# Kernel tuning notes

Measured on AMD Instinct MI355X. Metric: run time of the kernel, lower is better.

## Reference

```python
import jax, jax.numpy as jnp
import numpy as np

BATCH, FIELD0, EMB = 1024, 32, 64
LAYER_SIZES = (128, 128, 128)  # split_half=True -> hidden field sizes [32, 64, 64]


def setup_inputs() -> dict:
    key = jax.random.key(0)
    ks = jax.random.split(key, 7)
    x = jax.random.normal(ks[0], (BATCH, FIELD0, EMB), dtype=jnp.float32)
    # Conv1D(kernel_size=1) weights: (in_channels=f0*fi, filters=layer_size), plus bias.
    field_sizes = [FIELD0]
    params = {}
    for i, size in enumerate(LAYER_SIZES):
        fi = field_sizes[-1]
        fan_in = FIELD0 * fi
        scale = 1.0 / np.sqrt(fan_in)
        params[f"W{i}"] = jax.random.normal(ks[1 + 2 * i], (fan_in, size), dtype=jnp.float32) * scale
        params[f"b{i}"] = jnp.zeros((size,), dtype=jnp.float32)
        field_sizes.append(size // 2 if i != len(LAYER_SIZES) - 1 else size)
    return {"x": x, **params}


def reference(x, W0, b0, W1, b1, W2, b2):
    # CIN: outer product + 1x1 conv (a matmul over the flattened field-pair axis)
    # fused as a single bilinear contraction per layer:
    #   cur[b,k,e] = sum_{i,j} x[b,i,e] * hidden[b,j,e] * W[i,j,k] + b[k]
    Ws = [(W0, b0), (W1, b1), (W2, b2)]
    f0 = x.shape[1]
    hidden = x
    final_outputs = []
    n_layers = len(Ws)
    for idx, (W, b) in enumerate(Ws):
        fi = hidden.shape[1]
        Wr = W.reshape(f0, fi, W.shape[-1])  # channel m = i*fi + j (row-major reshape)
        cur = jnp.einsum('bie,bje,ijk->bke', x, hidden, Wr) + b[None, :, None]
        # activation=None -> linear
        if idx != n_layers - 1:
            half = cur.shape[1] // 2
            hidden, direct = cur[:, :half, :], cur[:, half:, :]
        else:
            direct = cur
        final_outputs.append(direct)
    result = jnp.concatenate(final_outputs, axis=1)  # (B, 64+64+128, E)
    return jnp.sum(result, axis=-1)  # (B, 256)
```

## Files before the change

kernel.cpp:

```cpp
#include <hip/hip_runtime.h>
#include <cstdint>


typedef _Float16 half8  __attribute__((ext_vector_type(8)));
typedef _Float16 half4_ __attribute__((ext_vector_type(4)));
typedef _Float16 half2_ __attribute__((ext_vector_type(2)));
typedef float    f32x4  __attribute__((ext_vector_type(4)));

__global__ void pack_w_all(const float* __restrict__ W0, _Float16* __restrict__ Wt0,
                           const float* __restrict__ W1, _Float16* __restrict__ Wt1,
                           const float* __restrict__ W2, _Float16* __restrict__ Wt2)
{
    __shared__ _Float16 ldsT[128 * 33];
    const int blk = blockIdx.x, t = threadIdx.x;
    const float* W;
    _Float16* Wt;
    int c, fi;
    if (blk < 32)       { W = W0; Wt = Wt0; c = blk;      fi = 32; }
    else if (blk < 96)  { W = W1; Wt = Wt1; c = blk - 32; fi = 64; }
    else                { W = W2; Wt = Wt2; c = blk - 96; fi = 64; }

    for (int p = t; p < 32 * 128; p += 256) {
        int kk = p >> 7, m = p & 127;
        ldsT[m * 33 + kk] = (_Float16)W[(size_t)(kk * fi + c) * 128 + m];
    }
    __syncthreads();
    int m = t >> 1, kk0 = (t & 1) * 16;
    half8 v0, v1;
#pragma unroll
    for (int i = 0; i < 8; ++i) {
        v0[i] = ldsT[m * 33 + kk0 + i];
        v1[i] = ldsT[m * 33 + kk0 + 8 + i];
    }
    *(half8*)(Wt + (size_t)c * 4096 + t * 16)     = v0;
    *(half8*)(Wt + (size_t)c * 4096 + t * 16 + 8) = v1;
}

template<int NCH>
__device__ __forceinline__ void kloop_t(f32x4 (&acc)[4][4],
    const _Float16* __restrict__ WtL, const _Float16* __restrict__ hB,
    const half8 (&xF)[4], int lr, int q)
{
#pragma unroll
    for (int mt = 0; mt < 4; ++mt)
#pragma unroll
        for (int nt = 0; nt < 4; ++nt)
            acc[mt][nt] = f32x4{0.0f, 0.0f, 0.0f, 0.0f};

    const _Float16* aG = WtL + lr * 32 + q * 8;

    half8 afA[4], afB[4];
    _Float16 xsA[4], xsB[4];

    auto pf = [&](half8* af, _Float16* xs, int cc) {
        const _Float16* ag = aG + (size_t)cc * 4096;
#pragma unroll
        for (int mt = 0; mt < 4; ++mt)
            af[mt] = *(const half8*)(ag + mt * 512);
#pragma unroll
        for (int nt = 0; nt < 4; ++nt)
            xs[nt] = hB[cc * 72 + nt * 16 + lr];
    };
    auto cp = [&](half8* af, _Float16* xs) {
        __builtin_amdgcn_s_setprio(1);
#pragma unroll
        for (int nt = 0; nt < 4; ++nt) {
            half2_ xv2 = {xs[nt], xs[nt]};
            half8 xv8 = __builtin_shufflevector(xv2, xv2, 0, 1, 0, 1, 0, 1, 0, 1);
            half8 bf = xF[nt] * xv8;
#pragma unroll
            for (int mt = 0; mt < 4; ++mt)
                acc[mt][nt] = __builtin_amdgcn_mfma_f32_16x16x32_f16(
                    af[mt], bf, acc[mt][nt], 0, 0, 0);
        }
        __builtin_amdgcn_s_setprio(0);
    };

    pf(afA, xsA, 0);
    for (int cc = 0; cc < NCH; cc += 2) {
        pf(afB, xsB, cc + 1);
        cp(afA, xsA);
        if (cc + 2 < NCH) pf(afA, xsA, cc + 2);
        cp(afB, xsB);
    }
}

__global__ __launch_bounds__(256, 2)
void cin_fused(const float* __restrict__ x,
               const _Float16* __restrict__ Wt0,
               const _Float16* __restrict__ Wt1,
               const float* __restrict__ bs0,
               const float* __restrict__ bs1,
               _Float16* __restrict__ S0,
               _Float16* __restrict__ S1,
               _Float16* __restrict__ S2)
{
    __shared__ alignas(16) char smem[57344];
    const int t = threadIdx.x, lane = t & 63, w = t >> 6;
    const int lr = lane & 15, q = lane >> 4;
    const int batch = blockIdx.x * 4 + w;

    _Float16* hB = (_Float16*)(smem + w * 14336);
    _Float16* xT = (_Float16*)(smem + w * 14336 + 9216);

    {
        const float4* xv = (const float4*)(x + (size_t)batch * 2048);
#pragma unroll
        for (int s = 0; s < 8; ++s) {
            int p4 = lane + s * 64;
            float4 v = xv[p4];
            int idx = p4 * 4, i = idx >> 6, e0 = idx & 63;
            _Float16 h0 = (_Float16)v.x, h1 = (_Float16)v.y;
            _Float16 h2 = (_Float16)v.z, h3 = (_Float16)v.w;
            half4_ pk = {h0, h1, h2, h3};
            *(half4_*)(hB + i * 72 + e0) = pk;
            xT[(e0 + 0) * 40 + i] = h0;
            xT[(e0 + 1) * 40 + i] = h1;
            xT[(e0 + 2) * 40 + i] = h2;
            xT[(e0 + 3) * 40 + i] = h3;
        }
    }

    half8 xF[4];
#pragma unroll
    for (int nt = 0; nt < 4; ++nt)
        xF[nt] = *(const half8*)(xT + (nt * 16 + lr) * 40 + q * 8);
    const half8 aF00 = *(const half8*)(hB + lr * 72 + q * 8);
    const half8 aF01 = *(const half8*)(hB + lr * 72 + q * 8 + 32);
    const half8 aF10 = *(const half8*)(hB + (16 + lr) * 72 + q * 8);
    const half8 aF11 = *(const half8*)(hB + (16 + lr) * 72 + q * 8 + 32);

    f32x4 acc[4][4];

    auto epi = [&](const float* bs) {
#pragma unroll
        for (int mt = 0; mt < 4; ++mt) {
            const int jb = mt * 16 + q * 4;
            const float b0f = bs[jb + 0], b1f = bs[jb + 1];
            const float b2f = bs[jb + 2], b3f = bs[jb + 3];
#pragma unroll
            for (int nt = 0; nt < 4; ++nt) {
                const int e = nt * 16 + lr;
                hB[(jb + 0) * 72 + e] = (_Float16)(acc[mt][nt][0] + b0f);
                hB[(jb + 1) * 72 + e] = (_Float16)(acc[mt][nt][1] + b1f);
                hB[(jb + 2) * 72 + e] = (_Float16)(acc[mt][nt][2] + b2f);
                hB[(jb + 3) * 72 + e] = (_Float16)(acc[mt][nt][3] + b3f);
            }
        }
    };

    auto sgemm = [&](int fi, _Float16* Sdst) {
        const int njt = fi >> 4;
        _Float16* Sb = Sdst + (size_t)batch * (32 * fi);
        for (int jt = 0; jt < njt; ++jt) {
            half8 bv0 = *(const half8*)(hB + (jt * 16 + lr) * 72 + q * 8);
            half8 bv1 = *(const half8*)(hB + (jt * 16 + lr) * 72 + q * 8 + 32);
            f32x4 sa = {0.0f, 0.0f, 0.0f, 0.0f};
            sa = __builtin_amdgcn_mfma_f32_16x16x32_f16(aF00, bv0, sa, 0, 0, 0);
            sa = __builtin_amdgcn_mfma_f32_16x16x32_f16(aF01, bv1, sa, 0, 0, 0);
            f32x4 sb = {0.0f, 0.0f, 0.0f, 0.0f};
            sb = __builtin_amdgcn_mfma_f32_16x16x32_f16(aF10, bv0, sb, 0, 0, 0);
            sb = __builtin_amdgcn_mfma_f32_16x16x32_f16(aF11, bv1, sb, 0, 0, 0);
            half4_ v0, v1;
#pragma unroll
            for (int r = 0; r < 4; ++r) { v0[r] = (_Float16)sa[r]; v1[r] = (_Float16)sb[r]; }
            *(half4_*)(Sb + (jt * 16 + lr) * 32 + q * 4)      = v0;
            *(half4_*)(Sb + (jt * 16 + lr) * 32 + 16 + q * 4) = v1;
        }
    };

    sgemm(32, S0);
    kloop_t<32>(acc, Wt0, hB, xF, lr, q);
    epi(bs0);
    sgemm(64, S1);
    kloop_t<64>(acc, Wt1, hB, xF, lr, q);
    epi(bs1);
    sgemm(64, S2);
}

__global__ __launch_bounds__(256, 2)
void cin_direct(const _Float16* __restrict__ S0v, const _Float16* __restrict__ S1v,
                const _Float16* __restrict__ S2v,
                const _Float16* __restrict__ Wt0, const _Float16* __restrict__ Wt1,
                const _Float16* __restrict__ Wt2,
                const float* __restrict__ bs0, const float* __restrict__ bs1,
                const float* __restrict__ bs2,
                float* __restrict__ out)
{
    __shared__ f32x4 red[3][64];
    const int t = threadIdx.x, lane = t & 63, kh = t >> 6;
    const int lr = lane & 15, q = lane >> 4;
    const int task = blockIdx.x;

    const _Float16 *S, *Wt;
    const float* bias;
    int fan, nch, dm0, ob, idx;
    if (task < 256)      { S = S0v; Wt = Wt0; bias = bs0; fan = 1024; nch = 32; dm0 = 64; ob = 0;   idx = task; }
    else if (task < 512) { S = S1v; Wt = Wt1; bias = bs1; fan = 2048; nch = 64; dm0 = 64; ob = 64;  idx = task - 256; }
    else                 { S = S2v; Wt = Wt2; bias = bs2; fan = 2048; nch = 64; dm0 = 0;  ob = 128; idx = task - 512; }
    const int bt = idx & 63, kt = idx >> 6;
    const int bbase = bt * 16;
    const int hq = nch >> 2, c0 = kh * hq;

    const _Float16* aG = Wt + (size_t)(dm0 + kt * 16 + lr) * 32 + q * 8
                            + (size_t)c0 * 4096;
    const _Float16* bG = S + (size_t)(bbase + lr) * fan + q * 8 + c0 * 32;

    f32x4 acc = {0.0f, 0.0f, 0.0f, 0.0f};
    half8 aA = *(const half8*)(aG);
    half8 bA = *(const half8*)(bG);
    for (int c = 0; c < hq; c += 2) {
        half8 aB = *(const half8*)(aG + (size_t)(c + 1) * 4096);
        half8 bB = *(const half8*)(bG + (c + 1) * 32);
        acc = __builtin_amdgcn_mfma_f32_16x16x32_f16(aA, bA, acc, 0, 0, 0);
        if (c + 2 < hq) {
            aA = *(const half8*)(aG + (size_t)(c + 2) * 4096);
            bA = *(const half8*)(bG + (c + 2) * 32);
        }
        acc = __builtin_amdgcn_mfma_f32_16x16x32_f16(aB, bB, acc, 0, 0, 0);
    }
    if (kh != 0) red[kh - 1][lane] = acc;
    __syncthreads();
    if (kh == 0) {
#pragma unroll
        for (int p = 0; p < 3; ++p) {
            f32x4 o = red[p][lane];
#pragma unroll
            for (int r = 0; r < 4; ++r) acc[r] += o[r];
        }
#pragma unroll
        for (int r = 0; r < 4; ++r) {
            int kl = kt * 16 + q * 4 + r;
            out[(size_t)(bbase + lr) * 256 + ob + kl]
                = acc[r] + 64.0f * bias[dm0 + kl];
        }
    }
}

extern "C" void kernel_launch(void* const* d_in, const int* in_sizes, int n_in,
                              void* d_out, int out_size, void* d_ws, size_t ws_size,
                              hipStream_t stream)
{
    const float* x  = (const float*)d_in[0];
    const float* W0 = (const float*)d_in[1];
    const float* b0 = (const float*)d_in[2];
    const float* W1 = (const float*)d_in[3];
    const float* b1 = (const float*)d_in[4];
    const float* W2 = (const float*)d_in[5];
    const float* b2 = (const float*)d_in[6];
    float* out = (float*)d_out;

    char* ws = (char*)d_ws;
    _Float16* Wt0 = (_Float16*)(ws + 0);
    _Float16* Wt1 = (_Float16*)(ws + 262144);
    _Float16* Wt2 = (_Float16*)(ws + 786432);
    _Float16* S0  = (_Float16*)(ws + 1310720);
    _Float16* S1  = (_Float16*)(ws + 3407872);
    _Float16* S2  = (_Float16*)(ws + 7602176);
    (void)in_sizes; (void)n_in; (void)out_size; (void)ws_size;

    hipLaunchKernelGGL(pack_w_all, dim3(160), dim3(256), 0, stream,
                       W0, Wt0, W1, Wt1, W2, Wt2);

    hipLaunchKernelGGL(cin_fused, dim3(256), dim3(256), 0, stream,
                       x, Wt0, Wt1, b0, b1, S0, S1, S2);

    hipLaunchKernelGGL(cin_direct, dim3(1024), dim3(256), 0, stream,
                       S0, S1, S2, Wt0, Wt1, Wt2, b0, b1, b2, out);
}
```

Before: 123.8 us.

## Split each batch's CIN recurrence across four waves with split-K LDS reduction

Before, each wave handled one batch element by itself. Now a whole 256-thread block handles one batch, and the grid grows from 256 to 1024 blocks. Each wave takes a quarter of the K channels in the hidden-layer GEMM, and the partial accumulators are summed through LDS in fp16 with several block barriers. The s-GEMM tiles are also spread across the waves. The aim is to raise parallelism and occupancy, since shared memory per block drops, at the cost of extra synchronisation and reduction traffic, plus some precision loss from fp16 partial sums.

After: 117.5 us. 1.05x faster.

```diff
diff --git a/kernel.cpp b/kernel.cpp
--- a/kernel.cpp
+++ b/kernel.cpp
@@ -39,7 +39,7 @@
 template<int NCH>
 __device__ __forceinline__ void kloop_t(f32x4 (&acc)[4][4],
     const _Float16* __restrict__ WtL, const _Float16* __restrict__ hB,
-    const half8 (&xF)[4], int lr, int q)
+    const half8 (&xF)[4], int lr, int q, int w)
 {
 #pragma unroll
     for (int mt = 0; mt < 4; ++mt)
@@ -47,7 +47,10 @@
         for (int nt = 0; nt < 4; ++nt)
             acc[mt][nt] = f32x4{0.0f, 0.0f, 0.0f, 0.0f};
 
-    const _Float16* aG = WtL + lr * 32 + q * 8;
+    constexpr int HC = NCH / 4;
+    const int c0 = w * HC;
+    const _Float16* aG = WtL + (size_t)c0 * 4096 + lr * 32 + q * 8;
+    const _Float16* hP = hB + (size_t)c0 * 72 + lr;
 
     half8 afA[4], afB[4];
     _Float16 xsA[4], xsB[4];
@@ -57,9 +60,10 @@
 #pragma unroll
         for (int mt = 0; mt < 4; ++mt)
             af[mt] = *(const half8*)(ag + mt * 512);
+        const _Float16* hh = hP + cc * 72;
 #pragma unroll
         for (int nt = 0; nt < 4; ++nt)
-            xs[nt] = hB[cc * 72 + nt * 16 + lr];
+            xs[nt] = hh[nt * 16];
     };
     auto cp = [&](half8* af, _Float16* xs) {
         __builtin_amdgcn_s_setprio(1);
@@ -77,10 +81,10 @@
     };
 
     pf(afA, xsA, 0);
-    for (int cc = 0; cc < NCH; cc += 2) {
+    for (int cc = 0; cc < HC; cc += 2) {
         pf(afB, xsB, cc + 1);
         cp(afA, xsA);
-        if (cc + 2 < NCH) pf(afA, xsA, cc + 2);
+        if (cc + 2 < HC) pf(afA, xsA, cc + 2);
         cp(afB, xsB);
     }
 }
@@ -95,19 +99,20 @@
                _Float16* __restrict__ S1,
                _Float16* __restrict__ S2)
 {
-    __shared__ alignas(16) char smem[57344];
+    __shared__ alignas(16) char smem[26624];
+    _Float16* xT   = (_Float16*)smem;
+    _Float16* hB   = (_Float16*)(smem + 5120);
+    _Float16* XC16 = (_Float16*)(smem + 14336);
+
     const int t = threadIdx.x, lane = t & 63, w = t >> 6;
     const int lr = lane & 15, q = lane >> 4;
-    const int batch = blockIdx.x * 4 + w;
-
-    _Float16* hB = (_Float16*)(smem + w * 14336);
-    _Float16* xT = (_Float16*)(smem + w * 14336 + 9216);
+    const int b = blockIdx.x;
 
     {
-        const float4* xv = (const float4*)(x + (size_t)batch * 2048);
-#pragma unroll
-        for (int s = 0; s < 8; ++s) {
-            int p4 = lane + s * 64;
+        const float4* xv = (const float4*)(x + (size_t)b * 2048);
+#pragma unroll
+        for (int s = 0; s < 2; ++s) {
+            int p4 = t + s * 256;
             float4 v = xv[p4];
             int idx = p4 * 4, i = idx >> 6, e0 = idx & 63;
             _Float16 h0 = (_Float16)v.x, h1 = (_Float16)v.y;
@@ -120,61 +125,103 @@
             xT[(e0 + 3) * 40 + i] = h3;
         }
     }
+    __syncthreads();
 
     half8 xF[4];
 #pragma unroll
     for (int nt = 0; nt < 4; ++nt)
         xF[nt] = *(const half8*)(xT + (nt * 16 + lr) * 40 + q * 8);
-    const half8 aF00 = *(const half8*)(hB + lr * 72 + q * 8);
-    const half8 aF01 = *(const half8*)(hB + lr * 72 + q * 8 + 32);
-    const half8 aF10 = *(const half8*)(hB + (16 + lr) * 72 + q * 8);
-    const half8 aF11 = *(const half8*)(hB + (16 + lr) * 72 + q * 8 + 32);
+    const int it = w & 1;
+    const half8 aF0 = *(const half8*)(hB + (it * 16 + lr) * 72 + q * 8);
+    const half8 aF1 = *(const half8*)(hB + (it * 16 + lr) * 72 + q * 8 + 32);
 
     f32x4 acc[4][4];
 
-    auto epi = [&](const float* bs) {
-#pragma unroll
-        for (int mt = 0; mt < 4; ++mt) {
-            const int jb = mt * 16 + q * 4;
-            const float b0f = bs[jb + 0], b1f = bs[jb + 1];
-            const float b2f = bs[jb + 2], b3f = bs[jb + 3];
-#pragma unroll
-            for (int nt = 0; nt < 4; ++nt) {
-                const int e = nt * 16 + lr;
-                hB[(jb + 0) * 72 + e] = (_Float16)(acc[mt][nt][0] + b0f);
-                hB[(jb + 1) * 72 + e] = (_Float16)(acc[mt][nt][1] + b1f);
-                hB[(jb + 2) * 72 + e] = (_Float16)(acc[mt][nt][2] + b2f);
-                hB[(jb + 3) * 72 + e] = (_Float16)(acc[mt][nt][3] + b3f);
+    auto xw_pair = [&](const f32x4 (&a)[4], int slot) {
+#pragma unroll
+        for (int cc = 0; cc < 2; ++cc) {
+            half8 hv8;
+#pragma unroll
+            for (int r = 0; r < 4; ++r) {
+                hv8[r]     = (_Float16)a[cc * 2][r];
+                hv8[4 + r] = (_Float16)a[cc * 2 + 1][r];
             }
-        }
+            *(half8*)(XC16 + slot * 1024 + cc * 512 + lane * 8) = hv8;
+        }
+    };
+    auto xr_sum = [&](f32x4 (&a)[4], int tgt) {
+#pragma unroll
+        for (int p = 0; p < 3; ++p) {
+#pragma unroll
+            for (int cc = 0; cc < 2; ++cc) {
+                half8 hv8 = *(const half8*)(XC16 + (tgt * 3 + p) * 1024
+                                            + cc * 512 + lane * 8);
+#pragma unroll
+                for (int r = 0; r < 4; ++r) {
+                    a[cc * 2][r]     += (float)hv8[r];
+                    a[cc * 2 + 1][r] += (float)hv8[4 + r];
+                }
+            }
+        }
+    };
+
+    auto epi_rows = [&](const f32x4 (&a)[4], const float* bs) {
+        const int jb = w * 16 + q * 4;
+        const float b0f = bs[jb + 0], b1f = bs[jb + 1];
+        const float b2f = bs[jb + 2], b3f = bs[jb + 3];
+#pragma unroll
+        for (int nt = 0; nt < 4; ++nt) {
+            const int e = nt * 16 + lr;
+            hB[(jb + 0) * 72 + e] = (_Float16)(a[nt][0] + b0f);
+            hB[(jb + 1) * 72 + e] = (_Float16)(a[nt][1] + b1f);
+            hB[(jb + 2) * 72 + e] = (_Float16)(a[nt][2] + b2f);
+            hB[(jb + 3) * 72 + e] = (_Float16)(a[nt][3] + b3f);
+        }
+    };
+
+    auto combine_epi = [&](const float* bs) {
+        if (w == 0)      { xw_pair(acc[1], 3); }
+        else if (w == 1) { xw_pair(acc[0], 0); }
+        else if (w == 2) { xw_pair(acc[0], 1); xw_pair(acc[1], 4); }
+        else             { xw_pair(acc[0], 2); xw_pair(acc[1], 5); }
+        __syncthreads();
+        if (w == 0)      { xr_sum(acc[0], 0); epi_rows(acc[0], bs); }
+        else if (w == 1) { xr_sum(acc[1], 1); epi_rows(acc[1], bs); }
+        __syncthreads();
+        if (w == 0)      { xw_pair(acc[2], 0); xw_pair(acc[3], 3); }
+        else if (w == 1) { xw_pair(acc[2], 1); xw_pair(acc[3], 4); }
+        else if (w == 2) { xw_pair(acc[3], 5); }
+        else             { xw_pair(acc[2], 2); }
+        __syncthreads();
+        if (w == 2)      { xr_sum(acc[2], 0); epi_rows(acc[2], bs); }
+        else if (w == 3) { xr_sum(acc[3], 1); epi_rows(acc[3], bs); }
     };
 
     auto sgemm = [&](int fi, _Float16* Sdst) {
-        const int njt = fi >> 4;
-        _Float16* Sb = Sdst + (size_t)batch * (32 * fi);
-        for (int jt = 0; jt < njt; ++jt) {
+        const int nT = fi >> 3;
+        _Float16* Sb = Sdst + (size_t)b * (32 * fi);
+        for (int tt = w; tt < nT; tt += 4) {
+            const int jt = tt >> 1;
+            f32x4 sa = {0.0f, 0.0f, 0.0f, 0.0f};
             half8 bv0 = *(const half8*)(hB + (jt * 16 + lr) * 72 + q * 8);
             half8 bv1 = *(const half8*)(hB + (jt * 16 + lr) * 72 + q * 8 + 32);
-            f32x4 sa = {0.0f, 0.0f, 0.0f, 0.0f};
-            sa = __builtin_amdgcn_mfma_f32_16x16x32_f16(aF00, bv0, sa, 0, 0, 0);
-            sa = __builtin_amdgcn_mfma_f32_16x16x32_f16(aF01, bv1, sa, 0, 0, 0);
-            f32x4 sb = {0.0f, 0.0f, 0.0f, 0.0f};
-            sb = __builtin_amdgcn_mfma_f32_16x16x32_f16(aF10, bv0, sb, 0, 0, 0);
-            sb = __builtin_amdgcn_mfma_f32_16x16x32_f16(aF11, bv1, sb, 0, 0, 0);
-            half4_ v0, v1;
-#pragma unroll
-            for (int r = 0; r < 4; ++r) { v0[r] = (_Float16)sa[r]; v1[r] = (_Float16)sb[r]; }
-            *(half4_*)(Sb + (jt * 16 + lr) * 32 + q * 4)      = v0;
-            *(half4_*)(Sb + (jt * 16 + lr) * 32 + 16 + q * 4) = v1;
+            sa = __builtin_amdgcn_mfma_f32_16x16x32_f16(aF0, bv0, sa, 0, 0, 0);
+            sa = __builtin_amdgcn_mfma_f32_16x16x32_f16(aF1, bv1, sa, 0, 0, 0);
+            half4_ v0;
+#pragma unroll
+            for (int r = 0; r < 4; ++r) v0[r] = (_Float16)sa[r];
+            *(half4_*)(Sb + (jt * 16 + lr) * 32 + it * 16 + q * 4) = v0;
         }
     };
 
     sgemm(32, S0);
-    kloop_t<32>(acc, Wt0, hB, xF, lr, q);
-    epi(bs0);
+    kloop_t<32>(acc, Wt0, hB, xF, lr, q, w);
+    combine_epi(bs0);
+    __syncthreads();
     sgemm(64, S1);
-    kloop_t<64>(acc, Wt1, hB, xF, lr, q);
-    epi(bs1);
+    kloop_t<64>(acc, Wt1, hB, xF, lr, q, w);
+    combine_epi(bs1);
+    __syncthreads();
     sgemm(64, S2);
 }
 
@@ -262,7 +309,7 @@
     hipLaunchKernelGGL(pack_w_all, dim3(160), dim3(256), 0, stream,
                        W0, Wt0, W1, Wt1, W2, Wt2);
 
-    hipLaunchKernelGGL(cin_fused, dim3(256), dim3(256), 0, stream,
+    hipLaunchKernelGGL(cin_fused, dim3(1024), dim3(256), 0, stream,
                        x, Wt0, Wt1, b0, b1, S0, S1, S2);
 
     hipLaunchKernelGGL(cin_direct, dim3(1024), dim3(256), 0, stream,
```
